# Kernel optimization log

Measured on AMD Instinct MI355X. Metric: run time of the kernel, lower is better.

## Reference

```python
import jax, jax.numpy as jnp
import numpy as np

HP = 64  # padded height (next pow2 of 56)
WP = 64  # padded width
H, W = 56, 56


def fwht(x):
    """Walsh-Hadamard transform along last axis (n must be power of 2)."""
    n = x.shape[-1]
    h = 1
    while h < n:
        xr = x.reshape(*x.shape[:-1], n // (2 * h), 2 * h)
        a = xr[..., :h]
        b = xr[..., h:]
        x = jnp.concatenate([a + b, a - b], axis=-1).reshape(*x.shape[:-1], n)
        h *= 2
    return x


def fwht_axis(x, axis):
    if axis == -1:
        return fwht(x)
    return jnp.swapaxes(fwht(jnp.swapaxes(x, -1, axis)), -1, axis)


def ifwht_axis(x, axis):
    n = x.shape[axis]
    return fwht_axis(x, axis) / n


def setup_inputs() -> dict:
    key = jax.random.key(0)
    k1, k2, k3, k4 = jax.random.split(key, 4)
    x = jax.random.normal(k1, (64, 128, H, W), dtype=jnp.float32)
    # per-pod 1x1 conv weights (pods, out_ch, in_ch), kaiming-ish scale
    conv_w = jax.random.normal(k2, (2, 128, 128), dtype=jnp.float32) / np.sqrt(128.0)
    v = jax.random.uniform(k3, (2, HP, WP), dtype=jnp.float32)
    T = jax.random.uniform(k4, (2, HP, WP), dtype=jnp.float32) / 10.0
    return {"x": x, "conv_w": conv_w, "v": v, "T": T}


def reference(x, conv_w, v, T):
    # pad spatial dims to power of 2 (pad right/bottom)
    f0 = jnp.pad(x, ((0, 0), (0, 0), (0, HP - H), (0, WP - W)))
    # 2D WHT
    f1 = fwht_axis(f0, -1)
    f2 = fwht_axis(f1, -2)
    # per-pod: elementwise gate v, 1x1 conv, soft-threshold; then sum over pods
    # f3: (P, B, Cin, HP, WP)
    f3 = v[:, None, None, :, :] * f2[None]
    f4 = jnp.einsum('pbihw,poi->pbohw', f3, conv_w)
    thr = jax.nn.relu(T)[:, None, None, :, :]
    f5 = jnp.sign(f4) * jax.nn.relu(jnp.abs(f4) - thr)
    f6 = f5.sum(axis=0)
    # inverse 2D WHT
    f7 = ifwht_axis(f6, -1)
    f8 = ifwht_axis(f7, -2)
    y = f8[..., :H, :W]
    return y + x  # residual
```

## Files before the change

### kernel.cpp

```cpp
#include <hip/hip_runtime.h>

typedef unsigned short u16;
typedef unsigned int u32;
typedef __attribute__((ext_vector_type(8))) __bf16 bf16x8;
typedef __attribute__((ext_vector_type(8))) unsigned short u16x8;
typedef __attribute__((ext_vector_type(2))) unsigned int u32x2;
typedef __attribute__((ext_vector_type(4))) float f32x4;

__device__ __forceinline__ u16 f2bf(float f) {
  u32 u = __builtin_bit_cast(u32, f);
  u += 0x7FFFu + ((u >> 16) & 1u);
  return (u16)(u >> 16);
}
__device__ __forceinline__ float bf2f(u16 h) {
  u32 u = ((u32)h) << 16;
  return __builtin_bit_cast(float, u);
}

template <int M>
__device__ __forceinline__ void bfly16(float r[16]) {
#pragma unroll
  for (int j = 0; j < 16; ++j)
    if ((j & M) == 0) {
      float a = r[j], b = r[j | M];
      r[j] = a + b;
      r[j | M] = a - b;
    }
}

__global__ __launch_bounds__(256) void k0_wcat(const float* __restrict__ cw,
                                               u16* __restrict__ wc) {
  const int i = blockIdx.x * 256 + threadIdx.x;
  const int j = i & 7;
  const int lr = (i >> 3) & 15;
  const int lq = (i >> 7) & 3;
  const int q = (i >> 9) & 3;
  const int fm = (i >> 11) & 1;
  const int wv = (i >> 12) & 3;
  const int fp = (i >> 14) & 1;
  const int row = fp * 128 + wv * 32 + fm * 16 + lr;
  const int k = q * 32 + lq * 8 + j;
  wc[i] = f2bf(cw[row * 128 + k]);
}

__global__ __launch_bounds__(256) void k1_fwht(const float* __restrict__ x,
                                               u16* __restrict__ f2) {
  __shared__ float lds[64 * 68];
  const int t = threadIdx.x;
  const int b = blockIdx.x >> 4;
  const int cg = blockIdx.x & 15;
  const int hA = t >> 2, wq = t & 3;
  const int hg = t >> 4, rB = t & 15;
  const int wC = t & 63, rr = t >> 6;
  const bool hok = hA < 56;
  u16x8 outv[16];

#pragma unroll
  for (int pp = 0; pp < 8; ++pp) {
    const float* xp = x + (size_t)(b * 128 + cg * 8 + pp) * 3136;
    float r[16];
#pragma unroll
    for (int c4 = 0; c4 < 4; ++c4) {
      const int w0 = wq * 16 + c4 * 4;
      if (hok && w0 < 56) {
        const float4 v4 = *(const float4*)(xp + hA * 56 + w0);
        r[c4 * 4 + 0] = v4.x; r[c4 * 4 + 1] = v4.y;
        r[c4 * 4 + 2] = v4.z; r[c4 * 4 + 3] = v4.w;
      } else {
        r[c4 * 4 + 0] = 0.f; r[c4 * 4 + 1] = 0.f;
        r[c4 * 4 + 2] = 0.f; r[c4 * 4 + 3] = 0.f;
      }
    }
    bfly16<1>(r); bfly16<2>(r); bfly16<4>(r); bfly16<8>(r);
    if (pp) __syncthreads();
#pragma unroll
    for (int c4 = 0; c4 < 4; ++c4)
      *(float4*)&lds[hA * 68 + wq * 16 + c4 * 4] =
          make_float4(r[c4 * 4 + 0], r[c4 * 4 + 1], r[c4 * 4 + 2], r[c4 * 4 + 3]);
    __syncthreads();
    float q[16];
#pragma unroll
    for (int k = 0; k < 4; ++k)
#pragma unroll
      for (int d = 0; d < 4; ++d)
        q[k * 4 + d] = lds[(hg * 4 + d) * 68 + k * 16 + rB];
    bfly16<4>(q); bfly16<8>(q); bfly16<1>(q); bfly16<2>(q);
#pragma unroll
    for (int k = 0; k < 4; ++k)
#pragma unroll
      for (int d = 0; d < 4; ++d)
        lds[(hg * 4 + d) * 68 + k * 16 + rB] = q[k * 4 + d];
    __syncthreads();
    float s[16];
#pragma unroll
    for (int j = 0; j < 16; ++j) s[j] = lds[(4 * j + rr) * 68 + wC];
    bfly16<1>(s); bfly16<2>(s); bfly16<4>(s); bfly16<8>(s);
#pragma unroll
    for (int j = 0; j < 16; ++j) outv[j][pp] = f2bf(s[j]);
  }
  u16* dst = f2 + ((size_t)(b * 16 + cg) << 15);
#pragma unroll
  for (int j = 0; j < 16; ++j) {
    const int pos = (4 * j + rr) * 64 + wC;
    *(u16x8*)(dst + (size_t)pos * 8) = outv[j];
  }
}

__global__ __launch_bounds__(256, 2) void k2_mix(u16* __restrict__ fg,
                                                 const u16* __restrict__ wc,
                                                 const float* __restrict__ vv,
                                                 const float* __restrict__ tt) {
  const int t = threadIdx.x;
  const int b = blockIdx.x >> 6;
  const int p0 = (blockIdx.x & 63) << 6;
  u16* fb = fg + ((size_t)b << 19);
  const int wv = t >> 6, l = t & 63, lr = l & 15, lq = l >> 4;

  bf16x8 bfr[4][4];
#pragma unroll
  for (int q = 0; q < 4; ++q)
#pragma unroll
    for (int fn = 0; fn < 4; ++fn)
      bfr[q][fn] = __builtin_bit_cast(
          bf16x8, *(const u16x8*)(fb + ((size_t)(4 * q + lq) << 15) +
                                  (size_t)(p0 + fn * 16 + lr) * 8));
  bf16x8 afr[4][2][2];
#pragma unroll
  for (int q = 0; q < 4; ++q)
#pragma unroll
    for (int fp = 0; fp < 2; ++fp)
#pragma unroll
      for (int fm = 0; fm < 2; ++fm) {
        const int frag_id = ((fp * 4 + wv) * 2 + fm) * 4 + q;
        afr[q][fp][fm] = __builtin_bit_cast(
            bf16x8, *(const u16x8*)(wc + (frag_id << 9) + l * 8));
      }
  float v0s[4], v1s[4], t0s[4], t1s[4];
#pragma unroll
  for (int fn = 0; fn < 4; ++fn) {
    const int pos = p0 + fn * 16 + lr;
    v0s[fn] = vv[pos];
    v1s[fn] = vv[4096 + pos];
    t0s[fn] = fmaxf(tt[pos], 0.f);
    t1s[fn] = fmaxf(tt[4096 + pos], 0.f);
  }

  f32x4 acc[2][2][4] = {};
#pragma unroll
  for (int q = 0; q < 4; ++q)
#pragma unroll
    for (int fn = 0; fn < 4; ++fn)
#pragma unroll
      for (int fp = 0; fp < 2; ++fp)
#pragma unroll
        for (int fm = 0; fm < 2; ++fm)
          acc[fp][fm][fn] = __builtin_amdgcn_mfma_f32_16x16x32_bf16(
              afr[q][fp][fm], bfr[q][fn], acc[fp][fm][fn], 0, 0, 0);

  __syncthreads();
#pragma unroll
  for (int fn = 0; fn < 4; ++fn) {
    const int pos = p0 + fn * 16 + lr;
#pragma unroll
    for (int fm = 0; fm < 2; ++fm) {
      u16 w[4];
#pragma unroll
      for (int rg = 0; rg < 4; ++rg) {
        const float z0 = v0s[fn] * acc[0][fm][fn][rg];
        const float z1 = v1s[fn] * acc[1][fm][fn][rg];
        const float s0v = copysignf(fmaxf(fabsf(z0) - t0s[fn], 0.f), z0);
        const float s1v = copysignf(fmaxf(fabsf(z1) - t1s[fn], 0.f), z1);
        w[rg] = f2bf(s0v + s1v);
      }
      const int og = wv * 4 + fm * 2 + (lq >> 1);
      u32x2 pk;
      pk[0] = (u32)w[0] | ((u32)w[1] << 16);
      pk[1] = (u32)w[2] | ((u32)w[3] << 16);
      *(u32x2*)(fb + ((size_t)og << 15) + (size_t)pos * 8 + (lq & 1) * 4) = pk;
    }
  }
}

__global__ __launch_bounds__(256) void k3_iwht(const u16* __restrict__ g,
                                               const float* __restrict__ x,
                                               float* __restrict__ y) {
  __shared__ float lds[64 * 68];
  const int t = threadIdx.x;
  const int b = blockIdx.x >> 4;
  const int og = blockIdx.x & 15;
  const u16* gb = g + ((size_t)(b * 16 + og) << 15);
  const int hA = t >> 2, wq = t & 3;
  const int hg = t >> 4, rB = t & 15;
  const int wC = t & 63, rr = t >> 6;
  u16x8 inv[16];
#pragma unroll
  for (int e = 0; e < 16; ++e)
    inv[e] = *(const u16x8*)(gb + (size_t)(hA * 64 + wq * 16 + e) * 8);

#pragma unroll
  for (int pp = 0; pp < 8; ++pp) {
    float r[16];
#pragma unroll
    for (int e = 0; e < 16; ++e) r[e] = bf2f(inv[e][pp]);
    bfly16<1>(r); bfly16<2>(r); bfly16<4>(r); bfly16<8>(r);
    if (pp) __syncthreads();
#pragma unroll
    for (int c4 = 0; c4 < 4; ++c4)
      *(float4*)&lds[hA * 68 + wq * 16 + c4 * 4] =
          make_float4(r[c4 * 4 + 0], r[c4 * 4 + 1], r[c4 * 4 + 2], r[c4 * 4 + 3]);
    __syncthreads();
    float q[16];
#pragma unroll
    for (int k = 0; k < 4; ++k)
#pragma unroll
      for (int d = 0; d < 4; ++d)
        q[k * 4 + d] = lds[(hg * 4 + d) * 68 + k * 16 + rB];
    bfly16<4>(q); bfly16<8>(q); bfly16<1>(q); bfly16<2>(q);
#pragma unroll
    for (int k = 0; k < 4; ++k)
#pragma unroll
      for (int d = 0; d < 4; ++d)
        lds[(hg * 4 + d) * 68 + k * 16 + rB] = q[k * 4 + d];
    __syncthreads();
    float s[16];
#pragma unroll
    for (int j = 0; j < 16; ++j) s[j] = lds[(4 * j + rr) * 68 + wC];
    bfly16<1>(s); bfly16<2>(s); bfly16<4>(s); bfly16<8>(s);
    if (wC < 56) {
      const size_t plane = (size_t)(b * 128 + og * 8 + pp) * 3136;
#pragma unroll
      for (int j = 0; j < 14; ++j) {
        const int h = 4 * j + rr;
        const size_t idx = plane + (size_t)(h * 56 + wC);
        y[idx] = x[idx] + s[j] * (1.f / 4096.f);
      }
    }
  }
}

extern "C" void kernel_launch(void* const* d_in, const int* in_sizes, int n_in,
                              void* d_out, int out_size, void* d_ws, size_t ws_size,
                              hipStream_t stream) {
  const float* x = (const float*)d_in[0];
  const float* cw = (const float*)d_in[1];
  const float* v = (const float*)d_in[2];
  const float* T = (const float*)d_in[3];
  float* y = (float*)d_out;

  u16* f2 = (u16*)d_ws;
  u16* wcat = (u16*)((char*)d_ws + 67108864);

  k0_wcat<<<128, 256, 0, stream>>>(cw, wcat);
  k1_fwht<<<1024, 256, 0, stream>>>(x, f2);
  k2_mix<<<4096, 256, 0, stream>>>(f2, wcat, v, T);
  k3_iwht<<<1024, 256, 0, stream>>>(f2, x, y);
}
```

Measured before the change: 124.6 us.

## Double-buffer LDS and prefetch next plane in WHT kernels

In the forward and inverse WHT kernels, the global loads for the next channel plane (x input, or the residual x in the inverse) are issued one iteration ahead into registers. The shared-memory tile is double-buffered so the barrier at the top of each iteration can be dropped. __syncthreads is replaced by an explicit lgkmcnt wait plus s_barrier, which does not wait on outstanding global loads. The aim is to hide global memory latency behind the butterfly and LDS work, at the cost of more registers and LDS per block. Launch bounds are also raised to request 4 blocks per SM.

```diff
diff --git a/kernel.cpp b/kernel.cpp
--- a/kernel.cpp
+++ b/kernel.cpp
@@ -15,6 +15,11 @@
 __device__ __forceinline__ float bf2f(u16 h) {
   u32 u = ((u32)h) << 16;
   return __builtin_bit_cast(float, u);
+}
+
+__device__ __forceinline__ void lds_barrier() {
+  asm volatile("s_waitcnt lgkmcnt(0)" ::: "memory");
+  __builtin_amdgcn_s_barrier();
 }
 
 template <int M>
@@ -43,9 +48,9 @@
   wc[i] = f2bf(cw[row * 128 + k]);
 }
 
-__global__ __launch_bounds__(256) void k1_fwht(const float* __restrict__ x,
-                                               u16* __restrict__ f2) {
-  __shared__ float lds[64 * 68];
+__global__ __launch_bounds__(256, 4) void k1_fwht(const float* __restrict__ x,
+                                                  u16* __restrict__ f2) {
+  __shared__ float lds[2][64 * 68];
   const int t = threadIdx.x;
   const int b = blockIdx.x >> 4;
   const int cg = blockIdx.x & 15;
@@ -53,47 +58,60 @@
   const int hg = t >> 4, rB = t & 15;
   const int wC = t & 63, rr = t >> 6;
   const bool hok = hA < 56;
+  const float* xbase = x + (size_t)(b * 128 + cg * 8) * 3136;
+  float4 ld[2][4];
   u16x8 outv[16];
 
 #pragma unroll
+  for (int c4 = 0; c4 < 4; ++c4) {
+    const int w0 = wq * 16 + c4 * 4;
+    float4 v4 = make_float4(0.f, 0.f, 0.f, 0.f);
+    if (hok && w0 < 56) v4 = *(const float4*)(xbase + hA * 56 + w0);
+    ld[0][c4] = v4;
+  }
+
+#pragma unroll
   for (int pp = 0; pp < 8; ++pp) {
-    const float* xp = x + (size_t)(b * 128 + cg * 8 + pp) * 3136;
+    if (pp < 7) {
+      const float* xp = xbase + (size_t)(pp + 1) * 3136;
+#pragma unroll
+      for (int c4 = 0; c4 < 4; ++c4) {
+        const int w0 = wq * 16 + c4 * 4;
+        float4 v4 = make_float4(0.f, 0.f, 0.f, 0.f);
+        if (hok && w0 < 56) v4 = *(const float4*)(xp + hA * 56 + w0);
+        ld[(pp + 1) & 1][c4] = v4;
+      }
+    }
     float r[16];
 #pragma unroll
     for (int c4 = 0; c4 < 4; ++c4) {
-      const int w0 = wq * 16 + c4 * 4;
-      if (hok && w0 < 56) {
-        const float4 v4 = *(const float4*)(xp + hA * 56 + w0);
-        r[c4 * 4 + 0] = v4.x; r[c4 * 4 + 1] = v4.y;
-        r[c4 * 4 + 2] = v4.z; r[c4 * 4 + 3] = v4.w;
-      } else {
-        r[c4 * 4 + 0] = 0.f; r[c4 * 4 + 1] = 0.f;
-        r[c4 * 4 + 2] = 0.f; r[c4 * 4 + 3] = 0.f;
-      }
+      r[c4 * 4 + 0] = ld[pp & 1][c4].x;
+      r[c4 * 4 + 1] = ld[pp & 1][c4].y;
+      r[c4 * 4 + 2] = ld[pp & 1][c4].z;
+      r[c4 * 4 + 3] = ld[pp & 1][c4].w;
     }
     bfly16<1>(r); bfly16<2>(r); bfly16<4>(r); bfly16<8>(r);
-    if (pp) __syncthreads();
 #pragma unroll
     for (int c4 = 0; c4 < 4; ++c4)
-      *(float4*)&lds[hA * 68 + wq * 16 + c4 * 4] =
+      *(float4*)&lds[pp & 1][hA * 68 + wq * 16 + c4 * 4] =
           make_float4(r[c4 * 4 + 0], r[c4 * 4 + 1], r[c4 * 4 + 2], r[c4 * 4 + 3]);
-    __syncthreads();
+    lds_barrier();
     float q[16];
 #pragma unroll
     for (int k = 0; k < 4; ++k)
 #pragma unroll
       for (int d = 0; d < 4; ++d)
-        q[k * 4 + d] = lds[(hg * 4 + d) * 68 + k * 16 + rB];
+        q[k * 4 + d] = lds[pp & 1][(hg * 4 + d) * 68 + k * 16 + rB];
     bfly16<4>(q); bfly16<8>(q); bfly16<1>(q); bfly16<2>(q);
 #pragma unroll
     for (int k = 0; k < 4; ++k)
 #pragma unroll
       for (int d = 0; d < 4; ++d)
-        lds[(hg * 4 + d) * 68 + k * 16 + rB] = q[k * 4 + d];
-    __syncthreads();
+        lds[pp & 1][(hg * 4 + d) * 68 + k * 16 + rB] = q[k * 4 + d];
+    lds_barrier();
     float s[16];
 #pragma unroll
-    for (int j = 0; j < 16; ++j) s[j] = lds[(4 * j + rr) * 68 + wC];
+    for (int j = 0; j < 16; ++j) s[j] = lds[pp & 1][(4 * j + rr) * 68 + wC];
     bfly16<1>(s); bfly16<2>(s); bfly16<4>(s); bfly16<8>(s);
 #pragma unroll
     for (int j = 0; j < 16; ++j) outv[j][pp] = f2bf(s[j]);
@@ -181,10 +199,10 @@
   }
 }
 
-__global__ __launch_bounds__(256) void k3_iwht(const u16* __restrict__ g,
-                                               const float* __restrict__ x,
-                                               float* __restrict__ y) {
-  __shared__ float lds[64 * 68];
+__global__ __launch_bounds__(256, 4) void k3_iwht(const u16* __restrict__ g,
+                                                  const float* __restrict__ x,
+                                                  float* __restrict__ y) {
+  __shared__ float lds[2][64 * 68];
   const int t = threadIdx.x;
   const int b = blockIdx.x >> 4;
   const int og = blockIdx.x & 15;
@@ -192,47 +210,58 @@
   const int hA = t >> 2, wq = t & 3;
   const int hg = t >> 4, rB = t & 15;
   const int wC = t & 63, rr = t >> 6;
+  const size_t plane0 = (size_t)(b * 128 + og * 8) * 3136;
   u16x8 inv[16];
 #pragma unroll
   for (int e = 0; e < 16; ++e)
     inv[e] = *(const u16x8*)(gb + (size_t)(hA * 64 + wq * 16 + e) * 8);
+  float xr[2][14];
+  if (wC < 56) {
+#pragma unroll
+    for (int j = 0; j < 14; ++j)
+      xr[0][j] = x[plane0 + (size_t)((4 * j + rr) * 56 + wC)];
+  }
 
 #pragma unroll
   for (int pp = 0; pp < 8; ++pp) {
+    if (pp < 7 && wC < 56) {
+      const size_t pl = plane0 + (size_t)(pp + 1) * 3136;
+#pragma unroll
+      for (int j = 0; j < 14; ++j)
+        xr[(pp + 1) & 1][j] = x[pl + (size_t)((4 * j + rr) * 56 + wC)];
+    }
     float r[16];
 #pragma unroll
     for (int e = 0; e < 16; ++e) r[e] = bf2f(inv[e][pp]);
     bfly16<1>(r); bfly16<2>(r); bfly16<4>(r); bfly16<8>(r);
-    if (pp) __syncthreads();
 #pragma unroll
     for (int c4 = 0; c4 < 4; ++c4)
-      *(float4*)&lds[hA * 68 + wq * 16 + c4 * 4] =
+      *(float4*)&lds[pp & 1][hA * 68 + wq * 16 + c4 * 4] =
           make_float4(r[c4 * 4 + 0], r[c4 * 4 + 1], r[c4 * 4 + 2], r[c4 * 4 + 3]);
-    __syncthreads();
+    lds_barrier();
     float q[16];
 #pragma unroll
     for (int k = 0; k < 4; ++k)
 #pragma unroll
       for (int d = 0; d < 4; ++d)
-        q[k * 4 + d] = lds[(hg * 4 + d) * 68 + k * 16 + rB];
+        q[k * 4 + d] = lds[pp & 1][(hg * 4 + d) * 68 + k * 16 + rB];
     bfly16<4>(q); bfly16<8>(q); bfly16<1>(q); bfly16<2>(q);
 #pragma unroll
     for (int k = 0; k < 4; ++k)
 #pragma unroll
       for (int d = 0; d < 4; ++d)
-        lds[(hg * 4 + d) * 68 + k * 16 + rB] = q[k * 4 + d];
-    __syncthreads();
+        lds[pp & 1][(hg * 4 + d) * 68 + k * 16 + rB] = q[k * 4 + d];
+    lds_barrier();
     float s[16];
 #pragma unroll
-    for (int j = 0; j < 16; ++j) s[j] = lds[(4 * j + rr) * 68 + wC];
+    for (int j = 0; j < 16; ++j) s[j] = lds[pp & 1][(4 * j + rr) * 68 + wC];
     bfly16<1>(s); bfly16<2>(s); bfly16<4>(s); bfly16<8>(s);
     if (wC < 56) {
-      const size_t plane = (size_t)(b * 128 + og * 8 + pp) * 3136;
+      const size_t plane = plane0 + (size_t)pp * 3136;
 #pragma unroll
       for (int j = 0; j < 14; ++j) {
-        const int h = 4 * j + rr;
-        const size_t idx = plane + (size_t)(h * 56 + wC);
-        y[idx] = x[idx] + s[j] * (1.f / 4096.f);
+        const size_t idx = plane + (size_t)((4 * j + rr) * 56 + wC);
+        y[idx] = xr[pp & 1][j] + s[j] * (1.f / 4096.f);
       }
     }
   }
```

Measured after the change: 250.6 us. +101.2%, slower.

## Restructure forward WHT: one wavefront per plane, register column transform, shuffle row transform

Applied to the files above, without the earlier changes.

The forward 2D Walsh-Hadamard kernel is reorganised so that each of 8 wavefronts owns one channel plane. Each lane loads a full 64-row column into registers, does the height-axis transform entirely in registers, and does the width-axis transform with cross-lane xor shuffles. This removes the per-channel LDS round trips and barriers of the old version. LDS is now used only to transpose the results into the channel-interleaved bf16 layout for coalesced stores. The cost is 64-float register arrays per thread and column-wise 4-byte global loads (coalesced across lanes), which may lower occupancy.

```diff
diff --git a/kernel.cpp b/kernel.cpp
--- a/kernel.cpp
+++ b/kernel.cpp
@@ -21,6 +21,16 @@
 __device__ __forceinline__ void bfly16(float r[16]) {
 #pragma unroll
   for (int j = 0; j < 16; ++j)
+    if ((j & M) == 0) {
+      float a = r[j], b = r[j | M];
+      r[j] = a + b;
+      r[j | M] = a - b;
+    }
+}
+template <int M>
+__device__ __forceinline__ void bfly64(float r[64]) {
+#pragma unroll
+  for (int j = 0; j < 64; ++j)
     if ((j & M) == 0) {
       float a = r[j], b = r[j | M];
       r[j] = a + b;
@@ -43,66 +53,49 @@
   wc[i] = f2bf(cw[row * 128 + k]);
 }
 
-__global__ __launch_bounds__(256) void k1_fwht(const float* __restrict__ x,
+__global__ __launch_bounds__(512) void k1_fwht(const float* __restrict__ x,
                                                u16* __restrict__ f2) {
-  __shared__ float lds[64 * 68];
+  __shared__ u16 lo[4096 * 8];
   const int t = threadIdx.x;
+  const int w = t & 63;
+  const int p = t >> 6;
   const int b = blockIdx.x >> 4;
   const int cg = blockIdx.x & 15;
-  const int hA = t >> 2, wq = t & 3;
-  const int hg = t >> 4, rB = t & 15;
-  const int wC = t & 63, rr = t >> 6;
-  const bool hok = hA < 56;
-  u16x8 outv[16];
-
-#pragma unroll
-  for (int pp = 0; pp < 8; ++pp) {
-    const float* xp = x + (size_t)(b * 128 + cg * 8 + pp) * 3136;
-    float r[16];
-#pragma unroll
-    for (int c4 = 0; c4 < 4; ++c4) {
-      const int w0 = wq * 16 + c4 * 4;
-      if (hok && w0 < 56) {
-        const float4 v4 = *(const float4*)(xp + hA * 56 + w0);
-        r[c4 * 4 + 0] = v4.x; r[c4 * 4 + 1] = v4.y;
-        r[c4 * 4 + 2] = v4.z; r[c4 * 4 + 3] = v4.w;
-      } else {
-        r[c4 * 4 + 0] = 0.f; r[c4 * 4 + 1] = 0.f;
-        r[c4 * 4 + 2] = 0.f; r[c4 * 4 + 3] = 0.f;
-      }
-    }
-    bfly16<1>(r); bfly16<2>(r); bfly16<4>(r); bfly16<8>(r);
-    if (pp) __syncthreads();
-#pragma unroll
-    for (int c4 = 0; c4 < 4; ++c4)
-      *(float4*)&lds[hA * 68 + wq * 16 + c4 * 4] =
-          make_float4(r[c4 * 4 + 0], r[c4 * 4 + 1], r[c4 * 4 + 2], r[c4 * 4 + 3]);
-    __syncthreads();
-    float q[16];
-#pragma unroll
-    for (int k = 0; k < 4; ++k)
-#pragma unroll
-      for (int d = 0; d < 4; ++d)
-        q[k * 4 + d] = lds[(hg * 4 + d) * 68 + k * 16 + rB];
-    bfly16<4>(q); bfly16<8>(q); bfly16<1>(q); bfly16<2>(q);
-#pragma unroll
-    for (int k = 0; k < 4; ++k)
-#pragma unroll
-      for (int d = 0; d < 4; ++d)
-        lds[(hg * 4 + d) * 68 + k * 16 + rB] = q[k * 4 + d];
-    __syncthreads();
-    float s[16];
-#pragma unroll
-    for (int j = 0; j < 16; ++j) s[j] = lds[(4 * j + rr) * 68 + wC];
-    bfly16<1>(s); bfly16<2>(s); bfly16<4>(s); bfly16<8>(s);
-#pragma unroll
-    for (int j = 0; j < 16; ++j) outv[j][pp] = f2bf(s[j]);
-  }
+  const float* xp = x + (size_t)(b * 128 + cg * 8 + p) * 3136;
+
+  float r[64];
+#pragma unroll
+  for (int h = 56; h < 64; ++h) r[h] = 0.f;
+  if (w < 56) {
+#pragma unroll
+    for (int h = 0; h < 56; ++h) r[h] = xp[h * 56 + w];
+  } else {
+#pragma unroll
+    for (int h = 0; h < 56; ++h) r[h] = 0.f;
+  }
+
+  bfly64<1>(r); bfly64<2>(r); bfly64<4>(r); bfly64<8>(r);
+  bfly64<16>(r); bfly64<32>(r);
+
+#define K1_WST(M)                                    \
+  {                                                  \
+    _Pragma("unroll") for (int h = 0; h < 64; ++h) { \
+      const float v = __shfl_xor(r[h], M, 64);       \
+      r[h] = (w & M) ? (v - r[h]) : (r[h] + v);      \
+    }                                                \
+  }
+  K1_WST(1) K1_WST(2) K1_WST(4) K1_WST(8) K1_WST(16) K1_WST(32)
+#undef K1_WST
+
+#pragma unroll
+  for (int h = 0; h < 64; ++h) lo[(h * 64 + w) * 8 + p] = f2bf(r[h]);
+  __syncthreads();
+
   u16* dst = f2 + ((size_t)(b * 16 + cg) << 15);
 #pragma unroll
-  for (int j = 0; j < 16; ++j) {
-    const int pos = (4 * j + rr) * 64 + wC;
-    *(u16x8*)(dst + (size_t)pos * 8) = outv[j];
+  for (int k = 0; k < 8; ++k) {
+    const int g = k * 512 + t;
+    *(u16x8*)(dst + (size_t)g * 8) = *(const u16x8*)&lo[g * 8];
   }
 }
 
@@ -251,7 +244,7 @@
   u16* wcat = (u16*)((char*)d_ws + 67108864);
 
   k0_wcat<<<128, 256, 0, stream>>>(cw, wcat);
-  k1_fwht<<<1024, 256, 0, stream>>>(x, f2);
+  k1_fwht<<<1024, 512, 0, stream>>>(x, f2);
   k2_mix<<<4096, 256, 0, stream>>>(f2, wcat, v, T);
   k3_iwht<<<1024, 256, 0, stream>>>(f2, x, y);
 }
```

Measured after the change: 133.2 us. 6.9% more time.

## Prefetch next channel plane and double-buffer LDS in forward WHT kernel

Applied to the files above, without the earlier changes.

The forward WHT kernel now loads the next channel's input plane into registers while the current one is transformed, and ping-pongs between two LDS buffers. This drops the barrier that guarded LDS reuse at the start of each iteration. The remaining barriers are replaced with a custom barrier that waits only on the LDS counter, so outstanding global prefetch loads are not drained. Launch bounds now request 2 blocks per CU, and the change costs doubled LDS and extra registers for the prefetch.

```diff
diff --git a/kernel.cpp b/kernel.cpp
--- a/kernel.cpp
+++ b/kernel.cpp
@@ -15,6 +15,11 @@
 __device__ __forceinline__ float bf2f(u16 h) {
   u32 u = ((u32)h) << 16;
   return __builtin_bit_cast(float, u);
+}
+
+__device__ __forceinline__ void lds_barrier() {
+  asm volatile("s_waitcnt lgkmcnt(0)" ::: "memory");
+  __builtin_amdgcn_s_barrier();
 }
 
 template <int M>
@@ -43,9 +48,9 @@
   wc[i] = f2bf(cw[row * 128 + k]);
 }
 
-__global__ __launch_bounds__(256) void k1_fwht(const float* __restrict__ x,
-                                               u16* __restrict__ f2) {
-  __shared__ float lds[64 * 68];
+__global__ __launch_bounds__(256, 2) void k1_fwht(const float* __restrict__ x,
+                                                  u16* __restrict__ f2) {
+  __shared__ float lds[2][64 * 68];
   const int t = threadIdx.x;
   const int b = blockIdx.x >> 4;
   const int cg = blockIdx.x & 15;
@@ -53,47 +58,59 @@
   const int hg = t >> 4, rB = t & 15;
   const int wC = t & 63, rr = t >> 6;
   const bool hok = hA < 56;
+  const float* xbase = x + (size_t)(b * 128 + cg * 8) * 3136;
+  float4 ld0[4], ld1[4];
   u16x8 outv[16];
 
 #pragma unroll
+  for (int c4 = 0; c4 < 4; ++c4) {
+    const int w0 = wq * 16 + c4 * 4;
+    float4 v4 = make_float4(0.f, 0.f, 0.f, 0.f);
+    if (hok && w0 < 56) v4 = *(const float4*)(xbase + hA * 56 + w0);
+    ld0[c4] = v4;
+  }
+
+#pragma unroll
   for (int pp = 0; pp < 8; ++pp) {
-    const float* xp = x + (size_t)(b * 128 + cg * 8 + pp) * 3136;
+    if (pp < 7) {
+      const float* xp = xbase + (size_t)(pp + 1) * 3136;
+#pragma unroll
+      for (int c4 = 0; c4 < 4; ++c4) {
+        const int w0 = wq * 16 + c4 * 4;
+        float4 v4 = make_float4(0.f, 0.f, 0.f, 0.f);
+        if (hok && w0 < 56) v4 = *(const float4*)(xp + hA * 56 + w0);
+        if (pp & 1) ld0[c4] = v4; else ld1[c4] = v4;
+      }
+    }
     float r[16];
 #pragma unroll
     for (int c4 = 0; c4 < 4; ++c4) {
-      const int w0 = wq * 16 + c4 * 4;
-      if (hok && w0 < 56) {
-        const float4 v4 = *(const float4*)(xp + hA * 56 + w0);
-        r[c4 * 4 + 0] = v4.x; r[c4 * 4 + 1] = v4.y;
-        r[c4 * 4 + 2] = v4.z; r[c4 * 4 + 3] = v4.w;
-      } else {
-        r[c4 * 4 + 0] = 0.f; r[c4 * 4 + 1] = 0.f;
-        r[c4 * 4 + 2] = 0.f; r[c4 * 4 + 3] = 0.f;
-      }
+      const float4 v4 = (pp & 1) ? ld1[c4] : ld0[c4];
+      r[c4 * 4 + 0] = v4.x; r[c4 * 4 + 1] = v4.y;
+      r[c4 * 4 + 2] = v4.z; r[c4 * 4 + 3] = v4.w;
     }
     bfly16<1>(r); bfly16<2>(r); bfly16<4>(r); bfly16<8>(r);
-    if (pp) __syncthreads();
 #pragma unroll
     for (int c4 = 0; c4 < 4; ++c4)
-      *(float4*)&lds[hA * 68 + wq * 16 + c4 * 4] =
+      *(float4*)&lds[pp & 1][hA * 68 + wq * 16 + c4 * 4] =
           make_float4(r[c4 * 4 + 0], r[c4 * 4 + 1], r[c4 * 4 + 2], r[c4 * 4 + 3]);
-    __syncthreads();
+    lds_barrier();
     float q[16];
 #pragma unroll
     for (int k = 0; k < 4; ++k)
 #pragma unroll
       for (int d = 0; d < 4; ++d)
-        q[k * 4 + d] = lds[(hg * 4 + d) * 68 + k * 16 + rB];
+        q[k * 4 + d] = lds[pp & 1][(hg * 4 + d) * 68 + k * 16 + rB];
     bfly16<4>(q); bfly16<8>(q); bfly16<1>(q); bfly16<2>(q);
 #pragma unroll
     for (int k = 0; k < 4; ++k)
 #pragma unroll
       for (int d = 0; d < 4; ++d)
-        lds[(hg * 4 + d) * 68 + k * 16 + rB] = q[k * 4 + d];
-    __syncthreads();
+        lds[pp & 1][(hg * 4 + d) * 68 + k * 16 + rB] = q[k * 4 + d];
+    lds_barrier();
     float s[16];
 #pragma unroll
-    for (int j = 0; j < 16; ++j) s[j] = lds[(4 * j + rr) * 68 + wC];
+    for (int j = 0; j < 16; ++j) s[j] = lds[pp & 1][(4 * j + rr) * 68 + wC];
     bfly16<1>(s); bfly16<2>(s); bfly16<4>(s); bfly16<8>(s);
 #pragma unroll
     for (int j = 0; j < 16; ++j) outv[j][pp] = f2bf(s[j]);
```

After: 125.9 us. Within noise of the previous version (+1.1%).
